# Kernel tuning notes

Measured on AMD Instinct MI355X. Metric: run time of the kernel, lower is better.

The kernel has to match this reference:

```python
import jax, jax.numpy as jnp
import numpy as np

N_NODES = 100000
N_EDGES = 1600000
NIN = 128
NOUT = 128


def setup_inputs() -> dict:
    key = jax.random.key(0)
    k1, k2, k3, k4, k5 = jax.random.split(key, 5)
    x = jax.random.normal(k1, (N_NODES, NIN), dtype=jnp.float32)
    edge_index = jax.random.randint(k2, (2, N_EDGES), 0, N_NODES, dtype=jnp.int32)
    edge_attr = jax.random.uniform(k3, (N_EDGES,), dtype=jnp.float32)
    # GCNConv linear weight (glorot-ish scale) and bias
    W = jax.random.normal(k4, (NIN, NOUT), dtype=jnp.float32) / np.sqrt(NIN)
    b = jnp.zeros((NOUT,), dtype=jnp.float32)
    return {"x": x, "edge_index": edge_index, "edge_attr": edge_attr, "W": W, "b": b}


def reference(x, edge_index, edge_attr, W, b):
    # PyG GCNConv: out = D^{-1/2} (A + I) D^{-1/2} X W + b
    # edge_attr is accepted by the wrapper's forward but ignored.
    N = x.shape[0]
    src, dst = edge_index[0], edge_index[1]
    # add self-loops
    loops = jnp.arange(N, dtype=edge_index.dtype)
    src = jnp.concatenate([src, loops])
    dst = jnp.concatenate([dst, loops])
    # degree over destination nodes (unit edge weights + self loops)
    deg = jax.ops.segment_sum(jnp.ones_like(dst, dtype=x.dtype), dst, num_segments=N)
    dinv = jnp.where(deg > 0, jax.lax.rsqrt(deg), 0.0)
    norm = dinv[src] * dinv[dst]  # [E + N]
    h = x @ W  # [N, NOUT] — project before aggregation (PyG order)
    msgs = h[src] * norm[:, None]  # [E + N, NOUT] gathered messages
    out = jax.ops.segment_sum(msgs, dst, num_segments=N) + b
    return out
```

## Files before the change

### kernel.cpp

```cpp
#include <hip/hip_runtime.h>
#include <hip/hip_bf16.h>


#define NIN 128
#define NOUT 128
#define NPART 8
#define G_GROUPS 98
#define MAXD 64
#define WPITCH 68

typedef __attribute__((ext_vector_type(8))) short short8;
typedef __attribute__((ext_vector_type(4))) float f32x4;
typedef __attribute__((ext_vector_type(4))) int   i32x4;
typedef __attribute__((ext_vector_type(4))) float f32x4v;

__device__ __forceinline__ float bf2f(unsigned short u) {
    unsigned v = ((unsigned)u) << 16;
    return __uint_as_float(v);
}
__device__ __forceinline__ unsigned short f2bf(float f) {
    unsigned u = __float_as_uint(f);
    unsigned r = 0x7FFFu + ((u >> 16) & 1u);
    return (unsigned short)((u + r) >> 16);
}

__global__ __launch_bounds__(256, 8) void k_build(const float* __restrict__ x,
                                                  const float* __restrict__ W,
                                                  const int* __restrict__ ei,
                                                  int* __restrict__ cnt,
                                                  int* __restrict__ adj,
                                                  unsigned short* __restrict__ h,
                                                  int E, int N, int gb) {
    __shared__ unsigned short Wt[128 * WPITCH];

    int grp = blockIdx.x >> 5;
    int s   = blockIdx.x & 31;

    if ((s & 15) >= 8) {
        int p = s & 7;
        int o = (s >> 4) & 1;
        int c = grp * 2 + o;
        int PS = (N + NPART - 1) / NPART;
        int lo = p * PS, hi = min(N, lo + PS);
        int nchunk = 2 * G_GROUPS;
        int chunkE = (((E + nchunk - 1) / nchunk) + 3) & ~3;
        int e0 = c * chunkE, e1 = min(E, e0 + chunkE);

        auto proc = [&](i32x4 s4, i32x4 d4) {
            #pragma unroll
            for (int k = 0; k < 4; k++) {
                int d = d4[k];
                if (d >= lo && d < hi) {
                    int pos = atomicAdd(&cnt[d], 1);
                    if (pos < MAXD) adj[(size_t)d * MAXD + pos] = s4[k];
                }
            }
        };

        int e = e0 + (int)threadIdx.x * 4;
        if (e < e1) {
            i32x4 s4 = __builtin_nontemporal_load((const i32x4*)(ei + e));
            i32x4 d4 = __builtin_nontemporal_load((const i32x4*)(ei + E + e));
            for (int en = e + 1024; en < e1; en += 1024) {
                i32x4 s4n = __builtin_nontemporal_load((const i32x4*)(ei + en));
                i32x4 d4n = __builtin_nontemporal_load((const i32x4*)(ei + E + en));
                proc(s4, d4);
                s4 = s4n; d4 = d4n;
            }
            proc(s4, d4);
        }
        return;
    }

    int rid = grp * 16 + (s & 7) + ((s >> 4) & 1) * 8;
    if (rid >= gb) return;

    int wave = threadIdx.x >> 6, lane = threadIdx.x & 63;
    int node_base = rid * 64 + wave * 16;
    bool active = node_base < N;
    int c = lane & 15, quad = lane >> 4;

    const f32x4v* xrow = (const f32x4v*)(x + (size_t)(node_base + c) * NIN + quad * 8);

    f32x4 acc[8];
    #pragma unroll
    for (int nt = 0; nt < 8; nt++) acc[nt] = (f32x4)(0.0f);

    for (int idx = threadIdx.x; idx < 64 * 128; idx += 256) {
        int kk = idx >> 7, n = idx & 127;
        Wt[n * WPITCH + kk] = f2bf(W[kk * 128 + n]);
    }
    __syncthreads();

    if (active) {
        short8 a0, a1;
        {
            f32x4v f0 = __builtin_nontemporal_load(xrow + 0);
            f32x4v f1 = __builtin_nontemporal_load(xrow + 1);
            f32x4v g0 = __builtin_nontemporal_load(xrow + 8);
            f32x4v g1 = __builtin_nontemporal_load(xrow + 9);
            a0[0]=(short)f2bf(f0[0]); a0[1]=(short)f2bf(f0[1]); a0[2]=(short)f2bf(f0[2]); a0[3]=(short)f2bf(f0[3]);
            a0[4]=(short)f2bf(f1[0]); a0[5]=(short)f2bf(f1[1]); a0[6]=(short)f2bf(f1[2]); a0[7]=(short)f2bf(f1[3]);
            a1[0]=(short)f2bf(g0[0]); a1[1]=(short)f2bf(g0[1]); a1[2]=(short)f2bf(g0[2]); a1[3]=(short)f2bf(g0[3]);
            a1[4]=(short)f2bf(g1[0]); a1[5]=(short)f2bf(g1[1]); a1[6]=(short)f2bf(g1[2]); a1[7]=(short)f2bf(g1[3]);
        }
        #pragma unroll
        for (int nt = 0; nt < 8; nt++) {
            const unsigned short* wp = &Wt[(nt * 16 + c) * WPITCH + quad * 8];
            short8 b0 = *(const short8*)(wp);
            short8 b1 = *(const short8*)(wp + 32);
            acc[nt] = __builtin_amdgcn_mfma_f32_16x16x32_bf16(a0, b0, acc[nt], 0, 0, 0);
            acc[nt] = __builtin_amdgcn_mfma_f32_16x16x32_bf16(a1, b1, acc[nt], 0, 0, 0);
        }
    }
    __syncthreads();

    for (int idx = threadIdx.x; idx < 64 * 128; idx += 256) {
        int kk = idx >> 7, n = idx & 127;
        Wt[n * WPITCH + kk] = f2bf(W[(kk + 64) * 128 + n]);
    }
    __syncthreads();

    if (active) {
        short8 a2, a3;
        {
            f32x4v f0 = __builtin_nontemporal_load(xrow + 16);
            f32x4v f1 = __builtin_nontemporal_load(xrow + 17);
            f32x4v g0 = __builtin_nontemporal_load(xrow + 24);
            f32x4v g1 = __builtin_nontemporal_load(xrow + 25);
            a2[0]=(short)f2bf(f0[0]); a2[1]=(short)f2bf(f0[1]); a2[2]=(short)f2bf(f0[2]); a2[3]=(short)f2bf(f0[3]);
            a2[4]=(short)f2bf(f1[0]); a2[5]=(short)f2bf(f1[1]); a2[6]=(short)f2bf(f1[2]); a2[7]=(short)f2bf(f1[3]);
            a3[0]=(short)f2bf(g0[0]); a3[1]=(short)f2bf(g0[1]); a3[2]=(short)f2bf(g0[2]); a3[3]=(short)f2bf(g0[3]);
            a3[4]=(short)f2bf(g1[0]); a3[5]=(short)f2bf(g1[1]); a3[6]=(short)f2bf(g1[2]); a3[7]=(short)f2bf(g1[3]);
        }
        #pragma unroll
        for (int nt = 0; nt < 8; nt++) {
            const unsigned short* wp = &Wt[(nt * 16 + c) * WPITCH + quad * 8];
            short8 b0 = *(const short8*)(wp);
            short8 b1 = *(const short8*)(wp + 32);
            acc[nt] = __builtin_amdgcn_mfma_f32_16x16x32_bf16(a2, b0, acc[nt], 0, 0, 0);
            acc[nt] = __builtin_amdgcn_mfma_f32_16x16x32_bf16(a3, b1, acc[nt], 0, 0, 0);
        }

        #pragma unroll
        for (int nt = 0; nt < 8; nt++) {
            #pragma unroll
            for (int r = 0; r < 4; r++) {
                int node = node_base + quad * 4 + r;
                h[(size_t)node * NOUT + nt * 16 + c] = f2bf(acc[nt][r]);
            }
        }
    }
}

__global__ __launch_bounds__(256) void k_scale(unsigned short* __restrict__ h,
                                               const int* __restrict__ cnt, int N) {
    int idx = blockIdx.x * 256 + threadIdx.x;
    int total = N * (NOUT / 8);
    if (idx >= total) return;
    int node = idx >> 4;
    float dv = rsqrtf((float)(cnt[node] + 1));
    uint4* hq = (uint4*)h;
    uint4 v = hq[idx];
    unsigned r[4] = { v.x, v.y, v.z, v.w };
    #pragma unroll
    for (int w = 0; w < 4; w++) {
        float lo = bf2f((unsigned short)(r[w] & 0xFFFF)) * dv;
        float hi = bf2f((unsigned short)(r[w] >> 16)) * dv;
        r[w] = (unsigned)f2bf(lo) | ((unsigned)f2bf(hi) << 16);
    }
    v.x = r[0]; v.y = r[1]; v.z = r[2]; v.w = r[3];
    hq[idx] = v;
}

__global__ __launch_bounds__(256) void k_agg(const unsigned short* __restrict__ h,
                                             const int* __restrict__ cnt,
                                             const int* __restrict__ adj,
                                             const float* __restrict__ bias,
                                             float* __restrict__ out, int N) {
    int sub = threadIdx.x & 31;
    int node = blockIdx.x * 8 + (threadIdx.x >> 5);
    if (node >= N) return;

    int degc = cnt[node];
    float dn = rsqrtf((float)(degc + 1));
    int e0 = node * MAXD;
    int e1 = e0 + min(degc, MAXD);

    const uint2* hp = (const uint2*)h;

    float a0, a1, a2, a3;
    {
        uint2 v = hp[(size_t)node * 32 + sub];
        a0 = bf2f((unsigned short)(v.x & 0xFFFF));
        a1 = bf2f((unsigned short)(v.x >> 16));
        a2 = bf2f((unsigned short)(v.y & 0xFFFF));
        a3 = bf2f((unsigned short)(v.y >> 16));
    }

    int e = e0;
    for (; e + 7 < e1; e += 8) {
        i32x4 sA = *(const i32x4*)(adj + e);
        i32x4 sB = *(const i32x4*)(adj + e + 4);
        uint2 v0 = hp[(size_t)sA[0] * 32 + sub];
        uint2 v1 = hp[(size_t)sA[1] * 32 + sub];
        uint2 v2 = hp[(size_t)sA[2] * 32 + sub];
        uint2 v3 = hp[(size_t)sA[3] * 32 + sub];
        uint2 v4 = hp[(size_t)sB[0] * 32 + sub];
        uint2 v5 = hp[(size_t)sB[1] * 32 + sub];
        uint2 v6 = hp[(size_t)sB[2] * 32 + sub];
        uint2 v7 = hp[(size_t)sB[3] * 32 + sub];
        a0 += bf2f((unsigned short)(v0.x & 0xFFFF)) + bf2f((unsigned short)(v1.x & 0xFFFF))
            + bf2f((unsigned short)(v2.x & 0xFFFF)) + bf2f((unsigned short)(v3.x & 0xFFFF))
            + bf2f((unsigned short)(v4.x & 0xFFFF)) + bf2f((unsigned short)(v5.x & 0xFFFF))
            + bf2f((unsigned short)(v6.x & 0xFFFF)) + bf2f((unsigned short)(v7.x & 0xFFFF));
        a1 += bf2f((unsigned short)(v0.x >> 16)) + bf2f((unsigned short)(v1.x >> 16))
            + bf2f((unsigned short)(v2.x >> 16)) + bf2f((unsigned short)(v3.x >> 16))
            + bf2f((unsigned short)(v4.x >> 16)) + bf2f((unsigned short)(v5.x >> 16))
            + bf2f((unsigned short)(v6.x >> 16)) + bf2f((unsigned short)(v7.x >> 16));
        a2 += bf2f((unsigned short)(v0.y & 0xFFFF)) + bf2f((unsigned short)(v1.y & 0xFFFF))
            + bf2f((unsigned short)(v2.y & 0xFFFF)) + bf2f((unsigned short)(v3.y & 0xFFFF))
            + bf2f((unsigned short)(v4.y & 0xFFFF)) + bf2f((unsigned short)(v5.y & 0xFFFF))
            + bf2f((unsigned short)(v6.y & 0xFFFF)) + bf2f((unsigned short)(v7.y & 0xFFFF));
        a3 += bf2f((unsigned short)(v0.y >> 16)) + bf2f((unsigned short)(v1.y >> 16))
            + bf2f((unsigned short)(v2.y >> 16)) + bf2f((unsigned short)(v3.y >> 16))
            + bf2f((unsigned short)(v4.y >> 16)) + bf2f((unsigned short)(v5.y >> 16))
            + bf2f((unsigned short)(v6.y >> 16)) + bf2f((unsigned short)(v7.y >> 16));
    }
    for (; e + 3 < e1; e += 4) {
        i32x4 sA = *(const i32x4*)(adj + e);
        uint2 v0 = hp[(size_t)sA[0] * 32 + sub];
        uint2 v1 = hp[(size_t)sA[1] * 32 + sub];
        uint2 v2 = hp[(size_t)sA[2] * 32 + sub];
        uint2 v3 = hp[(size_t)sA[3] * 32 + sub];
        a0 += bf2f((unsigned short)(v0.x & 0xFFFF)) + bf2f((unsigned short)(v1.x & 0xFFFF))
            + bf2f((unsigned short)(v2.x & 0xFFFF)) + bf2f((unsigned short)(v3.x & 0xFFFF));
        a1 += bf2f((unsigned short)(v0.x >> 16)) + bf2f((unsigned short)(v1.x >> 16))
            + bf2f((unsigned short)(v2.x >> 16)) + bf2f((unsigned short)(v3.x >> 16));
        a2 += bf2f((unsigned short)(v0.y & 0xFFFF)) + bf2f((unsigned short)(v1.y & 0xFFFF))
            + bf2f((unsigned short)(v2.y & 0xFFFF)) + bf2f((unsigned short)(v3.y & 0xFFFF));
        a3 += bf2f((unsigned short)(v0.y >> 16)) + bf2f((unsigned short)(v1.y >> 16))
            + bf2f((unsigned short)(v2.y >> 16)) + bf2f((unsigned short)(v3.y >> 16));
    }
    for (; e < e1; e++) {
        int s = adj[e];
        uint2 v = hp[(size_t)s * 32 + sub];
        a0 += bf2f((unsigned short)(v.x & 0xFFFF));
        a1 += bf2f((unsigned short)(v.x >> 16));
        a2 += bf2f((unsigned short)(v.y & 0xFFFF));
        a3 += bf2f((unsigned short)(v.y >> 16));
    }

    float4 b4 = ((const float4*)bias)[sub];
    f32x4 o;
    o[0] = a0 * dn + b4.x;
    o[1] = a1 * dn + b4.y;
    o[2] = a2 * dn + b4.z;
    o[3] = a3 * dn + b4.w;
    __builtin_nontemporal_store(o, (f32x4*)(out + (size_t)node * NOUT) + sub);
}

static inline size_t align256(size_t v) { return (v + 255) & ~(size_t)255; }

extern "C" void kernel_launch(void* const* d_in, const int* in_sizes, int n_in,
                              void* d_out, int out_size, void* d_ws, size_t ws_size,
                              hipStream_t stream) {
    const float* x  = (const float*)d_in[0];
    const int*   ei = (const int*)d_in[1];
    const float* W  = (const float*)d_in[3];
    const float* b  = (const float*)d_in[4];
    float*       out = (float*)d_out;

    int N = in_sizes[0] / NIN;
    int E = in_sizes[1] / 2;
    int gb = (N + 63) / 64;

    char* ws = (char*)d_ws;
    size_t o = 0;
    int*   cnt = (int*)(ws + o);   o += align256((size_t)N * 4);
    int*   adj = (int*)(ws + o);   o += align256((size_t)N * MAXD * 4);
    unsigned short* h = (unsigned short*)(ws + o); o += align256((size_t)N * NOUT * 2);
    (void)ws_size; (void)n_in; (void)out_size;

    hipMemsetAsync(cnt, 0, (size_t)N * 4, stream);
    k_build<<<32 * G_GROUPS, 256, 0, stream>>>(x, W, ei, cnt, adj, h, E, N, gb);
    k_scale<<<(N * (NOUT / 8) + 255) / 256, 256, 0, stream>>>(h, cnt, N);
    k_agg<<<(N + 7) / 8, 256, 0, stream>>>(h, cnt, adj, b, out, N);
}
```

Before: 284.3 us.

## Fold source-degree scaling into aggregation and drop separate scale kernel

Removes the k_scale pass that rescaled every row of h by its source node's dinv. The aggregation kernel now gathers cnt[src] for each neighbour, computes rsqrt on the fly, and accumulates with FMAs. The self term is scaled by the node's own dinv. This saves a full read-modify-write of h and one kernel launch, at the cost of an extra random 4-byte gather and an rsqrt per edge. The edge-list loop in the build kernel is also simplified to plain loads without software prefetch or nontemporal hints.

Result: faster. 258.0 us (-9.2%).

```diff
diff --git a/kernel.cpp b/kernel.cpp
--- a/kernel.cpp
+++ b/kernel.cpp
@@ -45,8 +45,9 @@
         int nchunk = 2 * G_GROUPS;
         int chunkE = (((E + nchunk - 1) / nchunk) + 3) & ~3;
         int e0 = c * chunkE, e1 = min(E, e0 + chunkE);
-
-        auto proc = [&](i32x4 s4, i32x4 d4) {
+        for (int e = e0 + (int)threadIdx.x * 4; e < e1; e += 1024) {
+            i32x4 s4 = *(const i32x4*)(ei + e);
+            i32x4 d4 = *(const i32x4*)(ei + E + e);
             #pragma unroll
             for (int k = 0; k < 4; k++) {
                 int d = d4[k];
@@ -55,19 +56,6 @@
                     if (pos < MAXD) adj[(size_t)d * MAXD + pos] = s4[k];
                 }
             }
-        };
-
-        int e = e0 + (int)threadIdx.x * 4;
-        if (e < e1) {
-            i32x4 s4 = __builtin_nontemporal_load((const i32x4*)(ei + e));
-            i32x4 d4 = __builtin_nontemporal_load((const i32x4*)(ei + E + e));
-            for (int en = e + 1024; en < e1; en += 1024) {
-                i32x4 s4n = __builtin_nontemporal_load((const i32x4*)(ei + en));
-                i32x4 d4n = __builtin_nontemporal_load((const i32x4*)(ei + E + en));
-                proc(s4, d4);
-                s4 = s4n; d4 = d4n;
-            }
-            proc(s4, d4);
         }
         return;
     }
@@ -153,26 +141,6 @@
     }
 }
 
-__global__ __launch_bounds__(256) void k_scale(unsigned short* __restrict__ h,
-                                               const int* __restrict__ cnt, int N) {
-    int idx = blockIdx.x * 256 + threadIdx.x;
-    int total = N * (NOUT / 8);
-    if (idx >= total) return;
-    int node = idx >> 4;
-    float dv = rsqrtf((float)(cnt[node] + 1));
-    uint4* hq = (uint4*)h;
-    uint4 v = hq[idx];
-    unsigned r[4] = { v.x, v.y, v.z, v.w };
-    #pragma unroll
-    for (int w = 0; w < 4; w++) {
-        float lo = bf2f((unsigned short)(r[w] & 0xFFFF)) * dv;
-        float hi = bf2f((unsigned short)(r[w] >> 16)) * dv;
-        r[w] = (unsigned)f2bf(lo) | ((unsigned)f2bf(hi) << 16);
-    }
-    v.x = r[0]; v.y = r[1]; v.z = r[2]; v.w = r[3];
-    hq[idx] = v;
-}
-
 __global__ __launch_bounds__(256) void k_agg(const unsigned short* __restrict__ h,
                                              const int* __restrict__ cnt,
                                              const int* __restrict__ adj,
@@ -192,16 +160,18 @@
     float a0, a1, a2, a3;
     {
         uint2 v = hp[(size_t)node * 32 + sub];
-        a0 = bf2f((unsigned short)(v.x & 0xFFFF));
-        a1 = bf2f((unsigned short)(v.x >> 16));
-        a2 = bf2f((unsigned short)(v.y & 0xFFFF));
-        a3 = bf2f((unsigned short)(v.y >> 16));
+        a0 = bf2f((unsigned short)(v.x & 0xFFFF)) * dn;
+        a1 = bf2f((unsigned short)(v.x >> 16)) * dn;
+        a2 = bf2f((unsigned short)(v.y & 0xFFFF)) * dn;
+        a3 = bf2f((unsigned short)(v.y >> 16)) * dn;
     }
 
     int e = e0;
     for (; e + 7 < e1; e += 8) {
         i32x4 sA = *(const i32x4*)(adj + e);
         i32x4 sB = *(const i32x4*)(adj + e + 4);
+        int c0 = cnt[sA[0]], c1 = cnt[sA[1]], c2 = cnt[sA[2]], c3 = cnt[sA[3]];
+        int c4 = cnt[sB[0]], c5 = cnt[sB[1]], c6 = cnt[sB[2]], c7 = cnt[sB[3]];
         uint2 v0 = hp[(size_t)sA[0] * 32 + sub];
         uint2 v1 = hp[(size_t)sA[1] * 32 + sub];
         uint2 v2 = hp[(size_t)sA[2] * 32 + sub];
@@ -210,45 +180,77 @@
         uint2 v5 = hp[(size_t)sB[1] * 32 + sub];
         uint2 v6 = hp[(size_t)sB[2] * 32 + sub];
         uint2 v7 = hp[(size_t)sB[3] * 32 + sub];
-        a0 += bf2f((unsigned short)(v0.x & 0xFFFF)) + bf2f((unsigned short)(v1.x & 0xFFFF))
-            + bf2f((unsigned short)(v2.x & 0xFFFF)) + bf2f((unsigned short)(v3.x & 0xFFFF))
-            + bf2f((unsigned short)(v4.x & 0xFFFF)) + bf2f((unsigned short)(v5.x & 0xFFFF))
-            + bf2f((unsigned short)(v6.x & 0xFFFF)) + bf2f((unsigned short)(v7.x & 0xFFFF));
-        a1 += bf2f((unsigned short)(v0.x >> 16)) + bf2f((unsigned short)(v1.x >> 16))
-            + bf2f((unsigned short)(v2.x >> 16)) + bf2f((unsigned short)(v3.x >> 16))
-            + bf2f((unsigned short)(v4.x >> 16)) + bf2f((unsigned short)(v5.x >> 16))
-            + bf2f((unsigned short)(v6.x >> 16)) + bf2f((unsigned short)(v7.x >> 16));
-        a2 += bf2f((unsigned short)(v0.y & 0xFFFF)) + bf2f((unsigned short)(v1.y & 0xFFFF))
-            + bf2f((unsigned short)(v2.y & 0xFFFF)) + bf2f((unsigned short)(v3.y & 0xFFFF))
-            + bf2f((unsigned short)(v4.y & 0xFFFF)) + bf2f((unsigned short)(v5.y & 0xFFFF))
-            + bf2f((unsigned short)(v6.y & 0xFFFF)) + bf2f((unsigned short)(v7.y & 0xFFFF));
-        a3 += bf2f((unsigned short)(v0.y >> 16)) + bf2f((unsigned short)(v1.y >> 16))
-            + bf2f((unsigned short)(v2.y >> 16)) + bf2f((unsigned short)(v3.y >> 16))
-            + bf2f((unsigned short)(v4.y >> 16)) + bf2f((unsigned short)(v5.y >> 16))
-            + bf2f((unsigned short)(v6.y >> 16)) + bf2f((unsigned short)(v7.y >> 16));
+        float d0 = rsqrtf((float)(c0 + 1)), d1 = rsqrtf((float)(c1 + 1));
+        float d2 = rsqrtf((float)(c2 + 1)), d3 = rsqrtf((float)(c3 + 1));
+        float d4 = rsqrtf((float)(c4 + 1)), d5 = rsqrtf((float)(c5 + 1));
+        float d6 = rsqrtf((float)(c6 + 1)), d7 = rsqrtf((float)(c7 + 1));
+        a0 = fmaf(bf2f((unsigned short)(v0.x & 0xFFFF)), d0, a0);
+        a1 = fmaf(bf2f((unsigned short)(v0.x >> 16)),    d0, a1);
+        a2 = fmaf(bf2f((unsigned short)(v0.y & 0xFFFF)), d0, a2);
+        a3 = fmaf(bf2f((unsigned short)(v0.y >> 16)),    d0, a3);
+        a0 = fmaf(bf2f((unsigned short)(v1.x & 0xFFFF)), d1, a0);
+        a1 = fmaf(bf2f((unsigned short)(v1.x >> 16)),    d1, a1);
+        a2 = fmaf(bf2f((unsigned short)(v1.y & 0xFFFF)), d1, a2);
+        a3 = fmaf(bf2f((unsigned short)(v1.y >> 16)),    d1, a3);
+        a0 = fmaf(bf2f((unsigned short)(v2.x & 0xFFFF)), d2, a0);
+        a1 = fmaf(bf2f((unsigned short)(v2.x >> 16)),    d2, a1);
+        a2 = fmaf(bf2f((unsigned short)(v2.y & 0xFFFF)), d2, a2);
+        a3 = fmaf(bf2f((unsigned short)(v2.y >> 16)),    d2, a3);
+        a0 = fmaf(bf2f((unsigned short)(v3.x & 0xFFFF)), d3, a0);
+        a1 = fmaf(bf2f((unsigned short)(v3.x >> 16)),    d3, a1);
+        a2 = fmaf(bf2f((unsigned short)(v3.y & 0xFFFF)), d3, a2);
+        a3 = fmaf(bf2f((unsigned short)(v3.y >> 16)),    d3, a3);
+        a0 = fmaf(bf2f((unsigned short)(v4.x & 0xFFFF)), d4, a0);
+        a1 = fmaf(bf2f((unsigned short)(v4.x >> 16)),    d4, a1);
+        a2 = fmaf(bf2f((unsigned short)(v4.y & 0xFFFF)), d4, a2);
+        a3 = fmaf(bf2f((unsigned short)(v4.y >> 16)),    d4, a3);
+        a0 = fmaf(bf2f((unsigned short)(v5.x & 0xFFFF)), d5, a0);
+        a1 = fmaf(bf2f((unsigned short)(v5.x >> 16)),    d5, a1);
+        a2 = fmaf(bf2f((unsigned short)(v5.y & 0xFFFF)), d5, a2);
+        a3 = fmaf(bf2f((unsigned short)(v5.y >> 16)),    d5, a3);
+        a0 = fmaf(bf2f((unsigned short)(v6.x & 0xFFFF)), d6, a0);
+        a1 = fmaf(bf2f((unsigned short)(v6.x >> 16)),    d6, a1);
+        a2 = fmaf(bf2f((unsigned short)(v6.y & 0xFFFF)), d6, a2);
+        a3 = fmaf(bf2f((unsigned short)(v6.y >> 16)),    d6, a3);
+        a0 = fmaf(bf2f((unsigned short)(v7.x & 0xFFFF)), d7, a0);
+        a1 = fmaf(bf2f((unsigned short)(v7.x >> 16)),    d7, a1);
+        a2 = fmaf(bf2f((unsigned short)(v7.y & 0xFFFF)), d7, a2);
+        a3 = fmaf(bf2f((unsigned short)(v7.y >> 16)),    d7, a3);
     }
     for (; e + 3 < e1; e += 4) {
         i32x4 sA = *(const i32x4*)(adj + e);
+        int c0 = cnt[sA[0]], c1 = cnt[sA[1]], c2 = cnt[sA[2]], c3 = cnt[sA[3]];
         uint2 v0 = hp[(size_t)sA[0] * 32 + sub];
         uint2 v1 = hp[(size_t)sA[1] * 32 + sub];
         uint2 v2 = hp[(size_t)sA[2] * 32 + sub];
         uint2 v3 = hp[(size_t)sA[3] * 32 + sub];
-        a0 += bf2f((unsigned short)(v0.x & 0xFFFF)) + bf2f((unsigned short)(v1.x & 0xFFFF))
-            + bf2f((unsigned short)(v2.x & 0xFFFF)) + bf2f((unsigned short)(v3.x & 0xFFFF));
-        a1 += bf2f((unsigned short)(v0.x >> 16)) + bf2f((unsigned short)(v1.x >> 16))
-            + bf2f((unsigned short)(v2.x >> 16)) + bf2f((unsigned short)(v3.x >> 16));
-        a2 += bf2f((unsigned short)(v0.y & 0xFFFF)) + bf2f((unsigned short)(v1.y & 0xFFFF))
-            + bf2f((unsigned short)(v2.y & 0xFFFF)) + bf2f((unsigned short)(v3.y & 0xFFFF));
-        a3 += bf2f((unsigned short)(v0.y >> 16)) + bf2f((unsigned short)(v1.y >> 16))
-            + bf2f((unsigned short)(v2.y >> 16)) + bf2f((unsigned short)(v3.y >> 16));
+        float d0 = rsqrtf((float)(c0 + 1)), d1 = rsqrtf((float)(c1 + 1));
+        float d2 = rsqrtf((float)(c2 + 1)), d3 = rsqrtf((float)(c3 + 1));
+        a0 = fmaf(bf2f((unsigned short)(v0.x & 0xFFFF)), d0, a0);
+        a1 = fmaf(bf2f((unsigned short)(v0.x >> 16)),    d0, a1);
+        a2 = fmaf(bf2f((unsigned short)(v0.y & 0xFFFF)), d0, a2);
+        a3 = fmaf(bf2f((unsigned short)(v0.y >> 16)),    d0, a3);
+        a0 = fmaf(bf2f((unsigned short)(v1.x & 0xFFFF)), d1, a0);
+        a1 = fmaf(bf2f((unsigned short)(v1.x >> 16)),    d1, a1);
+        a2 = fmaf(bf2f((unsigned short)(v1.y & 0xFFFF)), d1, a2);
+        a3 = fmaf(bf2f((unsigned short)(v1.y >> 16)),    d1, a3);
+        a0 = fmaf(bf2f((unsigned short)(v2.x & 0xFFFF)), d2, a0);
+        a1 = fmaf(bf2f((unsigned short)(v2.x >> 16)),    d2, a1);
+        a2 = fmaf(bf2f((unsigned short)(v2.y & 0xFFFF)), d2, a2);
+        a3 = fmaf(bf2f((unsigned short)(v2.y >> 16)),    d2, a3);
+        a0 = fmaf(bf2f((unsigned short)(v3.x & 0xFFFF)), d3, a0);
+        a1 = fmaf(bf2f((unsigned short)(v3.x >> 16)),    d3, a1);
+        a2 = fmaf(bf2f((unsigned short)(v3.y & 0xFFFF)), d3, a2);
+        a3 = fmaf(bf2f((unsigned short)(v3.y >> 16)),    d3, a3);
     }
     for (; e < e1; e++) {
         int s = adj[e];
+        float ds = rsqrtf((float)(cnt[s] + 1));
         uint2 v = hp[(size_t)s * 32 + sub];
-        a0 += bf2f((unsigned short)(v.x & 0xFFFF));
-        a1 += bf2f((unsigned short)(v.x >> 16));
-        a2 += bf2f((unsigned short)(v.y & 0xFFFF));
-        a3 += bf2f((unsigned short)(v.y >> 16));
+        a0 = fmaf(bf2f((unsigned short)(v.x & 0xFFFF)), ds, a0);
+        a1 = fmaf(bf2f((unsigned short)(v.x >> 16)),    ds, a1);
+        a2 = fmaf(bf2f((unsigned short)(v.y & 0xFFFF)), ds, a2);
+        a3 = fmaf(bf2f((unsigned short)(v.y >> 16)),    ds, a3);
     }
 
     float4 b4 = ((const float4*)bias)[sub];
@@ -284,6 +286,5 @@
 
     hipMemsetAsync(cnt, 0, (size_t)N * 4, stream);
     k_build<<<32 * G_GROUPS, 256, 0, stream>>>(x, W, ei, cnt, adj, h, E, N, gb);
-    k_scale<<<(N * (NOUT / 8) + 255) / 256, 256, 0, stream>>>(h, cnt, N);
     k_agg<<<(N + 7) / 8, 256, 0, stream>>>(h, cnt, adj, b, out, N);
 }
```
